# Optimization experiments

Hardware: AMD Instinct MI355X
Metric: run time of the kernel (lower is better)

## Reference

```python
import jax, jax.numpy as jnp
import numpy as np

N, E, G = 10000, 80000, 32
Z, C, B, H = 10, 128, 8, 64
R_MAX = 5.0
AVG_NEIGH = 16.0
L_OFF = [0, 1, 4, 9, 16]  # slice offsets for l = 0..3 blocks of the SH vector


def real_sh(u):
    # Real spherical harmonics up to l=3, 'component' normalization (sum_m Y_lm^2 = 2l+1)
    x, y, z = u[:, 0], u[:, 1], u[:, 2]
    s3, s5, s15 = 3.0 ** 0.5, 5.0 ** 0.5, 15.0 ** 0.5
    cols = [
        jnp.ones_like(x),
        s3 * x, s3 * y, s3 * z,
        s15 * x * y, s15 * y * z, (s5 / 2) * (3 * z ** 2 - 1),
        s15 * x * z, (s15 / 2) * (x ** 2 - y ** 2),
        (70.0 ** 0.5 / 4) * (3 * x ** 2 * y - y ** 3),
        105.0 ** 0.5 * x * y * z,
        (42.0 ** 0.5 / 4) * y * (5 * z ** 2 - 1),
        (7.0 ** 0.5 / 2) * (5 * z ** 3 - 3 * z),
        (42.0 ** 0.5 / 4) * x * (5 * z ** 2 - 1),
        (105.0 ** 0.5 / 2) * z * (x ** 2 - y ** 2),
        (70.0 ** 0.5 / 4) * (x ** 3 - 3 * x * y ** 2),
    ]
    return jnp.stack(cols, axis=-1)  # [E, 16]


def poly_cutoff(x, p=5):
    f = (1.0 - (p + 1) * (p + 2) / 2 * x ** p
         + p * (p + 2) * x ** (p + 1)
         - p * (p + 1) / 2 * x ** (p + 2))
    return f * (x < 1.0).astype(f.dtype)


def setup_inputs() -> dict:
    key = jax.random.key(0)
    ks = jax.random.split(key, 20)
    vectors = jax.random.normal(ks[0], (E, 3), dtype=jnp.float32) * 1.5
    elem = jax.random.randint(ks[1], (N,), 0, Z)
    node_attrs = jax.nn.one_hot(elem, Z, dtype=jnp.float32)
    edge_index = jax.random.randint(ks[2], (2, E), 0, N).astype(jnp.int64)
    batch = jnp.sort(jax.random.randint(ks[3], (N,), 0, G)).astype(jnp.int64)

    def init(k, shape, fan_in):
        return jax.random.normal(k, shape, dtype=jnp.float32) / np.sqrt(fan_in)

    return {
        "vectors": vectors,
        "node_attrs": node_attrs,
        "W_embed": init(ks[4], (Z, C), Z),
        "atomic_energies": -jnp.arange(1, Z + 1, dtype=jnp.float32),
        "rw1": init(ks[5], (2, B, H), B),
        "rw2": init(ks[6], (2, H, H), H),
        "rw3": init(ks[7], (2, H, H), H),
        "rw4": init(ks[8], (2, H, 4 * C), H),
        "Wmix": init(ks[9], (2, 4, C, C), C),
        "U": init(ks[10], (2, Z, 4), Z),
        "Wprod": init(ks[11], (2, C, C), C),
        "Wsc": init(ks[12], (2, C, C), C),
        "Wro0": init(ks[13], (C, 1), C),
        "Wro1a": init(ks[14], (C, 16), C),
        "Wro1b": init(ks[15], (16, 1), 16),
        "scale": jnp.array([1.0], dtype=jnp.float32),
        "shift": jnp.array([0.0], dtype=jnp.float32),
        "edge_index": edge_index,
        "batch": batch,
    }


def reference(vectors, node_attrs, W_embed, atomic_energies, rw1, rw2, rw3, rw4,
              Wmix, U, Wprod, Wsc, Wro0, Wro1a, Wro1b, scale, shift,
              edge_index, batch):
    sender, receiver = edge_index[0], edge_index[1]
    r = jnp.linalg.norm(vectors, axis=-1)                     # [E]
    u = vectors / r[:, None]
    Y = real_sh(u)                                            # [E, 16]
    n = jnp.arange(1, B + 1, dtype=vectors.dtype)
    bessel = jnp.sqrt(2.0 / R_MAX) * jnp.sin(n[None] * jnp.pi * r[:, None] / R_MAX) / r[:, None]
    edge_feats = bessel * poly_cutoff(r / R_MAX)[:, None]     # [E, B]

    h = node_attrs @ W_embed                                  # [N, C] node embedding
    node_e0 = node_attrs @ atomic_energies                    # [N] atomic reference energies
    e0 = jax.ops.segment_sum(node_e0, batch, num_segments=G)  # [G]

    node_inter = jnp.zeros((node_attrs.shape[0],), dtype=vectors.dtype)
    for i in range(2):  # interaction layers (fixed small count)
        f = jax.nn.silu(edge_feats @ rw1[i])
        f = jax.nn.silu(f @ rw2[i])
        f = jax.nn.silu(f @ rw3[i])
        R_w = (f @ rw4[i]).reshape(-1, 4, C)                  # [E, 4, C] radial weights per l-path
        hs = h[sender]                                        # [E, C] edge gather
        A_parts = []
        for l in range(4):
            # channelwise tensor product (uvu): scalar node feats x Y_l -> l
            m = (R_w[:, l, :] * hs)[:, :, None] * Y[:, None, L_OFF[l]:L_OFF[l + 1]]  # [E, C, 2l+1]
            agg = jax.ops.segment_sum(m, receiver, num_segments=node_attrs.shape[0]) / AVG_NEIGH
            A_parts.append(jnp.einsum('ncm,cd->ndm', agg, Wmix[i, l]))
        # product basis: rotation-invariant powers per l, element-dependent contraction
        inv = jnp.stack([(p ** 2).sum(-1) for p in A_parts], axis=-1)  # [N, C, 4]
        w = node_attrs @ U[i]                                          # [N, 4]
        h = jnp.einsum('ncl,nl->nc', inv, w) @ Wprod[i] + h @ Wsc[i]   # product + residual sc
        if i == 0:
            node_inter = node_inter + (h @ Wro0)[:, 0]                 # linear readout
        else:
            node_inter = node_inter + (jax.nn.silu(h @ Wro1a) @ Wro1b)[:, 0]  # nonlinear readout
    node_inter = scale[0] * node_inter + shift[0]                       # scale-shift
    total = e0 + jax.ops.segment_sum(node_inter, batch, num_segments=G)
    return total  # [G] per-graph energies
```

## Files before the change

kernel.cpp:

```cpp
#include <hip/hip_runtime.h>

#define NN 10000
#define NE 80000
#define NG 32
#define NZ 10
#define NC 128
#define RMAXF 5.0f

typedef _Float16 f16;
typedef _Float16 half8 __attribute__((ext_vector_type(8)));
typedef float f32x4 __attribute__((ext_vector_type(4)));

__device__ __forceinline__ float silu_f(float x) {
    return x / (1.0f + __expf(-x));
}

__device__ __forceinline__ int clampi(int v, int lo, int hi) {
    return v < lo ? lo : (v > hi ? hi : v);
}

__device__ __forceinline__ uint4 pack8f(float4 a, float4 b) {
    union { f16 h[8]; uint4 u; } P;
    P.h[0] = (f16)a.x; P.h[1] = (f16)a.y; P.h[2] = (f16)a.z; P.h[3] = (f16)a.w;
    P.h[4] = (f16)b.x; P.h[5] = (f16)b.y; P.h[6] = (f16)b.z; P.h[7] = (f16)b.w;
    return P.u;
}

__global__ void zero_stuff(int* counts, int* cursor, float* out) {
    int i = blockIdx.x * blockDim.x + threadIdx.x;
    if (i < NN) { counts[i] = 0; cursor[i] = 0; }
    if (i < NG) out[i] = 0.0f;
}

__global__ void prep_weights(const float* __restrict__ Wmix, const float* __restrict__ Wprod,
                             const float* __restrict__ Wsc,
                             const float* __restrict__ rw2, const float* __restrict__ rw3,
                             const float* __restrict__ rw4,
                             f16* __restrict__ WmixT, f16* __restrict__ WprodT, f16* __restrict__ WscT,
                             f16* __restrict__ w2T, f16* __restrict__ w3T, f16* __restrict__ w4T) {
    int i = blockIdx.x * blockDim.x + threadIdx.x;
    if (i < 2 * 4 * 128 * 128) {
        int cc = i & 127, d = (i >> 7) & 127, g = i >> 14;
        WmixT[i] = (f16)Wmix[((size_t)g * 128 + cc) * 128 + d];
    }
    if (i < 2 * 128 * 128) {
        int cc = i & 127, d = (i >> 7) & 127, g = i >> 14;
        WprodT[i] = (f16)Wprod[((size_t)g * 128 + cc) * 128 + d];
        WscT[i]   = (f16)Wsc[((size_t)g * 128 + cc) * 128 + d];
    }
    if (i < 2 * 512 * 64) {
        int k = i & 63, j = (i >> 6) & 511, ly = i >> 15;
        w4T[i] = (f16)rw4[((size_t)ly * 64 + k) * 512 + j];
    }
    if (i < 2 * 64 * 64) {
        int k = i & 63, j = (i >> 6) & 63, ly = i >> 12;
        w2T[i] = (f16)rw2[((size_t)ly * 64 + k) * 64 + j];
        w3T[i] = (f16)rw3[((size_t)ly * 64 + k) * 64 + j];
    }
}

__global__ void node_init(const float* __restrict__ attrs, const float* __restrict__ W_embed,
                          const float* __restrict__ ae, const float* __restrict__ U,
                          float* __restrict__ h, float* __restrict__ node_e0, float* __restrict__ wU) {
    int gid = blockIdx.x * blockDim.x + threadIdx.x;
    if (gid >= NN * NC) return;
    int n = gid >> 7, c = gid & 127;
    float a[NZ];
#pragma unroll
    for (int z = 0; z < NZ; z++) a[z] = attrs[n * NZ + z];
    float acc = 0.f;
#pragma unroll
    for (int z = 0; z < NZ; z++) acc += a[z] * W_embed[z * NC + c];
    h[(size_t)n * NC + c] = acc;
    if (c == 0) {
        float e = 0.f;
#pragma unroll
        for (int z = 0; z < NZ; z++) e += a[z] * ae[z];
        node_e0[n] = e;
    }
    if (c < 8) {
        int i = c >> 2, l = c & 3;
        float s = 0.f;
#pragma unroll
        for (int z = 0; z < NZ; z++) s += a[z] * U[i * NZ * 4 + z * 4 + l];
        wU[(size_t)i * NN * 4 + n * 4 + l] = s;
    }
}

__global__ void edge_geom(const float* __restrict__ vec, float* __restrict__ Y, float* __restrict__ ef) {
    int e = blockIdx.x * blockDim.x + threadIdx.x;
    if (e >= NE) return;
    float vx = vec[e * 3 + 0], vy = vec[e * 3 + 1], vz = vec[e * 3 + 2];
    float r = sqrtf(vx * vx + vy * vy + vz * vz);
    float inv = 1.0f / r;
    float x = vx * inv, y = vy * inv, z = vz * inv;
    const float s3 = 1.7320508075688772f;
    const float s5 = 2.23606797749979f;
    const float s15 = 3.872983346207417f;
    const float c9 = 2.091650066335189f;
    const float c10 = 10.246950765959598f;
    const float c11 = 1.6201851746019651f;
    const float c12 = 1.3228756555322954f;
    const float c14 = 5.123475382979799f;
    float o[16];
    o[0] = 1.0f;
    o[1] = s3 * x; o[2] = s3 * y; o[3] = s3 * z;
    o[4] = s15 * x * y; o[5] = s15 * y * z; o[6] = 0.5f * s5 * (3.f * z * z - 1.f);
    o[7] = s15 * x * z; o[8] = 0.5f * s15 * (x * x - y * y);
    o[9] = c9 * (3.f * x * x * y - y * y * y);
    o[10] = c10 * x * y * z;
    o[11] = c11 * y * (5.f * z * z - 1.f);
    o[12] = c12 * (5.f * z * z * z - 3.f * z);
    o[13] = c11 * x * (5.f * z * z - 1.f);
    o[14] = c14 * z * (x * x - y * y);
    o[15] = c9 * (x * x * x - 3.f * x * y * y);
#pragma unroll
    for (int m = 0; m < 16; m++) Y[(size_t)e * 16 + m] = o[m];
    float xc = r / RMAXF;
    float cut = 0.0f;
    if (xc < 1.0f) {
        float x5 = xc * xc * xc * xc * xc;
        cut = 1.0f - 21.0f * x5 + 35.0f * x5 * xc - 15.0f * x5 * xc * xc;
    }
    float pref = sqrtf(2.0f / RMAXF) * inv * cut;
#pragma unroll
    for (int b = 0; b < 8; b++) {
        float arg = (float)(b + 1) * 3.14159265358979323846f * r / RMAXF;
        ef[(size_t)e * 8 + b] = pref * sinf(arg);
    }
}

__global__ void hist_recv(const int* __restrict__ recv, int* __restrict__ counts) {
    int e = blockIdx.x * blockDim.x + threadIdx.x;
    if (e < NE) atomicAdd(&counts[clampi(recv[e], 0, NN - 1)], 1);
}

__global__ void scan_counts(const int* __restrict__ counts, int* __restrict__ rowstart) {
    __shared__ int part[1024];
    int t = threadIdx.x;
    const int CH = 10;
    int base = t * CH;
    int loc[CH];
    int s = 0;
#pragma unroll
    for (int j = 0; j < CH; j++) {
        int v = (base + j < NN) ? counts[base + j] : 0;
        loc[j] = s; s += v;
    }
    part[t] = s;
    __syncthreads();
    for (int off = 1; off < 1024; off <<= 1) {
        int v = (t >= off) ? part[t - off] : 0;
        __syncthreads();
        part[t] += v;
        __syncthreads();
    }
    int chunk = (t > 0) ? part[t - 1] : 0;
#pragma unroll
    for (int j = 0; j < CH; j++)
        if (base + j < NN) rowstart[base + j] = chunk + loc[j];
    if (t == 0) rowstart[NN] = part[1023];
}

__global__ void scatter_edges(const int* __restrict__ recv, const int* __restrict__ rowstart,
                              int* __restrict__ cursor, int* __restrict__ elist) {
    int e = blockIdx.x * blockDim.x + threadIdx.x;
    if (e < NE) {
        int r = clampi(recv[e], 0, NN - 1);
        int p = atomicAdd(&cursor[r], 1);
        int slot = clampi(rowstart[r] + p, 0, NE - 1);
        elist[slot] = e;
    }
}

__global__ __launch_bounds__(256) void edge_mlp(const float* __restrict__ ef,
                                                const float* __restrict__ w1,
                                                const f16* __restrict__ w2T, const f16* __restrict__ w3T,
                                                const f16* __restrict__ w4T,
                                                f16* __restrict__ Rw) {
    __shared__ __align__(16) char L[16384];
    char* X1 = L;
    char* X2 = L + 8192;

    int tid = threadIdx.x;
    int lane = tid & 63;
    int w = tid >> 6;
    int ln = lane & 15, kq = lane >> 4;
    int eb = blockIdx.x * 64;

    {
        int jb = w * 16;
        const float4* efv = (const float4*)(ef + (size_t)(eb + lane) * 8);
        float4 ea = efv[0], eb4 = efv[1];
        float in8[8] = {ea.x, ea.y, ea.z, ea.w, eb4.x, eb4.y, eb4.z, eb4.w};
        f16 pk[16];
#pragma unroll
        for (int j = 0; j < 16; j++) {
            float a = 0.f;
#pragma unroll
            for (int b = 0; b < 8; b++) a += in8[b] * w1[b * 64 + jb + j];
            pk[j] = (f16)silu_f(a);
        }
        int base = lane * 128 + jb * 2;
#pragma unroll
        for (int t = 0; t < 2; t++) {
            int byte = (base + t * 16) ^ ((lane & 7) << 4);
            *(uint4*)(X1 + byte) = ((uint4*)pk)[t];
        }
    }
    __syncthreads();

    {
        half8 a[2];
#pragma unroll
        for (int kc = 0; kc < 2; kc++) {
            int row = w * 16 + ln;
            int byte = (row * 128 + kc * 64 + kq * 16) ^ ((row & 7) << 4);
            a[kc] = *(const half8*)(X1 + byte);
        }
#pragma unroll
        for (int nt = 0; nt < 4; nt++) {
            f32x4 acc = {0.f, 0.f, 0.f, 0.f};
#pragma unroll
            for (int kc = 0; kc < 2; kc++) {
                half8 b = *(const half8*)(w2T + (nt * 16 + ln) * 64 + kc * 32 + kq * 8);
                acc = __builtin_amdgcn_mfma_f32_16x16x32_f16(a[kc], b, acc, 0, 0, 0);
            }
#pragma unroll
            for (int r = 0; r < 4; r++) {
                int row = w * 16 + kq * 4 + r;
                int byte = (row * 128 + (nt * 16 + ln) * 2) ^ ((row & 7) << 4);
                *(f16*)(X2 + byte) = (f16)silu_f(acc[r]);
            }
        }
    }
    __syncthreads();

    {
        half8 a[2];
#pragma unroll
        for (int kc = 0; kc < 2; kc++) {
            int row = w * 16 + ln;
            int byte = (row * 128 + kc * 64 + kq * 16) ^ ((row & 7) << 4);
            a[kc] = *(const half8*)(X2 + byte);
        }
#pragma unroll
        for (int nt = 0; nt < 4; nt++) {
            f32x4 acc = {0.f, 0.f, 0.f, 0.f};
#pragma unroll
            for (int kc = 0; kc < 2; kc++) {
                half8 b = *(const half8*)(w3T + (nt * 16 + ln) * 64 + kc * 32 + kq * 8);
                acc = __builtin_amdgcn_mfma_f32_16x16x32_f16(a[kc], b, acc, 0, 0, 0);
            }
#pragma unroll
            for (int r = 0; r < 4; r++) {
                int row = w * 16 + kq * 4 + r;
                int byte = (row * 128 + (nt * 16 + ln) * 2) ^ ((row & 7) << 4);
                *(f16*)(X1 + byte) = (f16)silu_f(acc[r]);
            }
        }
    }
    __syncthreads();

    half8 a3[2];
#pragma unroll
    for (int kc = 0; kc < 2; kc++) {
        int row = w * 16 + ln;
        int byte = (row * 128 + kc * 64 + kq * 16) ^ ((row & 7) << 4);
        a3[kc] = *(const half8*)(X1 + byte);
    }
    for (int s = 0; s < 8; s++) {
#pragma unroll
        for (int nt = 0; nt < 4; nt++) {
            f32x4 acc = {0.f, 0.f, 0.f, 0.f};
#pragma unroll
            for (int kc = 0; kc < 2; kc++) {
                half8 b = *(const half8*)(w4T + (s * 64 + nt * 16 + ln) * 64 + kc * 32 + kq * 8);
                acc = __builtin_amdgcn_mfma_f32_16x16x32_f16(a3[kc], b, acc, 0, 0, 0);
            }
#pragma unroll
            for (int r = 0; r < 4; r++) {
                int row = w * 16 + kq * 4 + r;
                int byte = (row * 128 + (nt * 16 + ln) * 2) ^ ((row & 7) << 4);
                *(f16*)(X2 + byte) = (f16)acc[r];
            }
        }
        __syncthreads();
#pragma unroll
        for (int it = 0; it < 2; it++) {
            int i = it * 256 + tid;
            int row = i >> 3, chunk = i & 7;
            int byte = (row * 128 + chunk * 16) ^ ((row & 7) << 4);
            uint4 v = *(const uint4*)(X2 + byte);
            *(uint4*)(Rw + (size_t)(eb + row) * 512 + s * 64 + chunk * 8) = v;
        }
        __syncthreads();
    }
}

__global__ __launch_bounds__(256) void agg_only(const int* __restrict__ rowstart, const int* __restrict__ elist,
                                                const int* __restrict__ send, const float* __restrict__ h_in,
                                                const f16* __restrict__ Rw, const float* __restrict__ Y,
                                                f16* __restrict__ aggH) {
    __shared__ int eL[64], sL[64];
    int n = blockIdx.x, tid = threadIdx.x;
    int c = tid & 127, mh = tid >> 7;
    float acc[8];
#pragma unroll
    for (int q = 0; q < 8; q++) acc[q] = 0.f;
    int beg = rowstart[n], end = rowstart[n + 1];
    for (int base = beg; base < end; base += 64) {
        int cnt = min(64, end - base);
        __syncthreads();
        if (tid < cnt) {
            int e = clampi(elist[base + tid], 0, NE - 1);
            eL[tid] = e;
            sL[tid] = clampi(send[e], 0, NN - 1);
        }
        __syncthreads();
        for (int idx = 0; idx < cnt; idx++) {
            int e = eL[idx];
            int s = sL[idx];
            float hs = h_in[(size_t)s * NC + c];
            const f16* rwp = Rw + (size_t)e * 512;
            float y[8];
#pragma unroll
            for (int q = 0; q < 8; q++) y[q] = Y[(size_t)e * 16 + mh * 8 + q];
            if (mh == 0) {
                float p0 = (float)rwp[c] * hs;
                float p1 = (float)rwp[128 + c] * hs;
                float p2 = (float)rwp[256 + c] * hs;
                acc[0] += p0 * y[0];
                acc[1] += p1 * y[1]; acc[2] += p1 * y[2]; acc[3] += p1 * y[3];
                acc[4] += p2 * y[4]; acc[5] += p2 * y[5]; acc[6] += p2 * y[6]; acc[7] += p2 * y[7];
            } else {
                float p2 = (float)rwp[256 + c] * hs;
                float p3 = (float)rwp[384 + c] * hs;
                acc[0] += p2 * y[0];
#pragma unroll
                for (int q = 1; q < 8; q++) acc[q] += p3 * y[q];
            }
        }
    }
    const float inv16 = 1.0f / 16.0f;
#pragma unroll
    for (int q = 0; q < 8; q++)
        aggH[(size_t)n * 2048 + (size_t)(mh * 8 + q) * NC + c] = (f16)(acc[q] * inv16);
}

__global__ __launch_bounds__(256) void mix_a(
    const f16* __restrict__ aggH, const f16* __restrict__ WmixT,
    const float* __restrict__ wU, f16* __restrict__ invwG, int layer)
{
    __shared__ __align__(16) char Lb[16384];

    int tid = threadIdx.x;
    int b = blockIdx.x;
    int nb = (b >> 1) * 16;
    int half = b & 1;
    int lane = tid & 63;
    int w = tid >> 6;
    int dt = half * 4 + w;
    int ln = lane & 15, kq = lane >> 4;
    char* myB = Lb + w * 4096;

    float4 wUreg[4];
#pragma unroll
    for (int r = 0; r < 4; r++)
        wUreg[r] = *(const float4*)(wU + (size_t)(nb + kq * 4 + r) * 4);

    float invwacc[4] = {0.f, 0.f, 0.f, 0.f};
    const f16* aggRow = aggH + (size_t)(nb + ln) * 2048 + kq * 8;

#pragma unroll
    for (int g = 0; g < 4; g++) {
        const int mstart = (g == 0) ? 0 : (g == 1) ? 1 : (g == 2) ? 4 : 9;
        const int mend   = (g == 0) ? 1 : (g == 1) ? 4 : (g == 2) ? 9 : 16;
        {
            const f16* Bt = WmixT + ((size_t)(layer * 4 + g) << 14);
#pragma unroll
            for (int i = 0; i < 4; i++) {
                int q = i * 64 + lane;
                int row = q >> 4, col = q & 15;
                uint4 v = *(const uint4*)(Bt + (dt * 16 + row) * 128 + col * 8);
                int byte = (row * 256 + col * 16) ^ ((row & 7) << 4);
                *(uint4*)(myB + byte) = v;
            }
        }
#pragma unroll
        for (int m = mstart; m < mend; m++) {
            f32x4 acc = {0.f, 0.f, 0.f, 0.f};
#pragma unroll
            for (int k = 0; k < 4; k++) {
                half8 a = *(const half8*)(aggRow + m * 128 + k * 32);
                int byte = (ln * 256 + k * 64 + kq * 16) ^ ((ln & 7) << 4);
                half8 bb = *(const half8*)(myB + byte);
                acc = __builtin_amdgcn_mfma_f32_16x16x32_f16(a, bb, acc, 0, 0, 0);
            }
#pragma unroll
            for (int r = 0; r < 4; r++) {
                float wur = (g == 0) ? wUreg[r].x : (g == 1) ? wUreg[r].y : (g == 2) ? wUreg[r].z : wUreg[r].w;
                invwacc[r] += acc[r] * acc[r] * wur;
            }
        }
    }

#pragma unroll
    for (int r = 0; r < 4; r++)
        invwG[(size_t)(nb + kq * 4 + r) * 128 + dt * 16 + ln] = (f16)invwacc[r];
}

__global__ __launch_bounds__(512) void mix_b(
    const f16* __restrict__ invwG, const float* __restrict__ h_in,
    const f16* __restrict__ WprodT, const f16* __restrict__ WscT,
    const float* __restrict__ Wro0, const float* __restrict__ Wro1a, const float* __restrict__ Wro1b,
    float* __restrict__ h_out, float* __restrict__ ni, int layer)
{
    __shared__ __align__(16) char Lb[13312];
    f16*   invwH = (f16*)(Lb);
    f16*   hH    = (f16*)(Lb + 4096);
    f16*   houtH = (f16*)(Lb + 8192);
    float* p16L  = (float*)(Lb + 12288);

    int tid = threadIdx.x;
    int nb = blockIdx.x * 16;
    int lane = tid & 63;
    int w = tid >> 6;
    int ln = lane & 15, kq = lane >> 4;

    if (tid < 256) {
        int node = tid >> 4, ch = tid & 15;
        int byte = (node * 256 + ch * 16) ^ ((node & 7) << 4);
        uint4 iv = *(const uint4*)(invwG + (size_t)(nb + node) * 128 + ch * 8);
        *(uint4*)((char*)invwH + byte) = iv;
        const float4* hp = (const float4*)(h_in + (size_t)(nb + node) * 128 + ch * 8);
        float4 g0 = hp[0], g1 = hp[1];
        *(uint4*)((char*)hH + byte) = pack8f(g0, g1);
    }
    __syncthreads();

    {
        half8 ai[4], ah[4];
#pragma unroll
        for (int k = 0; k < 4; k++) {
            int byte = (ln * 256 + (k * 32 + kq * 8) * 2) ^ ((ln & 7) << 4);
            ai[k] = *(const half8*)((char*)invwH + byte);
            ah[k] = *(const half8*)((char*)hH + byte);
        }
        const f16* Bp = WprodT + ((size_t)layer << 14);
        const f16* Bs = WscT + ((size_t)layer << 14);
        f32x4 acc = {0.f, 0.f, 0.f, 0.f};
#pragma unroll
        for (int k = 0; k < 4; k++) {
            half8 bb = *(const half8*)(Bp + (w * 16 + ln) * 128 + k * 32 + kq * 8);
            acc = __builtin_amdgcn_mfma_f32_16x16x32_f16(ai[k], bb, acc, 0, 0, 0);
        }
#pragma unroll
        for (int k = 0; k < 4; k++) {
            half8 bb = *(const half8*)(Bs + (w * 16 + ln) * 128 + k * 32 + kq * 8);
            acc = __builtin_amdgcn_mfma_f32_16x16x32_f16(ah[k], bb, acc, 0, 0, 0);
        }
#pragma unroll
        for (int r = 0; r < 4; r++) {
            int node = kq * 4 + r;
            int d = w * 16 + ln;
            h_out[(size_t)(nb + node) * 128 + d] = acc[r];
            houtH[node * 128 + d] = (f16)acc[r];
        }
    }
    __syncthreads();

    if (tid < 256) {
        int rn = tid >> 4, rj = tid & 15;
        if (layer == 0) {
            float s = 0.f;
            for (int cc = rj; cc < 128; cc += 16) s += (float)houtH[rn * 128 + cc] * Wro0[cc];
            p16L[tid] = s;
        } else {
            float s = 0.f;
            for (int cc = 0; cc < 128; cc++) s += (float)houtH[rn * 128 + cc] * Wro1a[cc * 16 + rj];
            s = silu_f(s);
            p16L[tid] = s * Wro1b[rj];
        }
    }
    __syncthreads();
    if (tid < 16) {
        float t = 0.f;
#pragma unroll
        for (int j = 0; j < 16; j++) t += p16L[tid * 16 + j];
        ni[nb + tid] = (layer == 0) ? t : (ni[nb + tid] + t);
    }
}

__global__ void finalize(const float* __restrict__ node_e0, const float* __restrict__ ni,
                         const int* __restrict__ batch, const float* __restrict__ scale,
                         const float* __restrict__ shift, float* __restrict__ out) {
    __shared__ float bins[NG];
    int tid = threadIdx.x;
    if (tid < NG) bins[tid] = 0.f;
    __syncthreads();
    int n = blockIdx.x * blockDim.x + tid;
    if (n < NN) {
        float v = node_e0[n] + scale[0] * ni[n] + shift[0];
        atomicAdd(&bins[clampi(batch[n], 0, NG - 1)], v);
    }
    __syncthreads();
    if (tid < NG) atomicAdd(&out[tid], bins[tid]);
}

extern "C" void kernel_launch(void* const* d_in, const int* in_sizes, int n_in,
                              void* d_out, int out_size, void* d_ws, size_t ws_size,
                              hipStream_t stream) {
    (void)in_sizes; (void)n_in; (void)out_size; (void)ws_size;
    const float* vectors = (const float*)d_in[0];
    const float* attrs   = (const float*)d_in[1];
    const float* W_embed = (const float*)d_in[2];
    const float* ae      = (const float*)d_in[3];
    const float* rw1     = (const float*)d_in[4];
    const float* rw2     = (const float*)d_in[5];
    const float* rw3     = (const float*)d_in[6];
    const float* rw4     = (const float*)d_in[7];
    const float* Wmix    = (const float*)d_in[8];
    const float* U       = (const float*)d_in[9];
    const float* Wprod   = (const float*)d_in[10];
    const float* Wsc     = (const float*)d_in[11];
    const float* Wro0    = (const float*)d_in[12];
    const float* Wro1a   = (const float*)d_in[13];
    const float* Wro1b   = (const float*)d_in[14];
    const float* scale   = (const float*)d_in[15];
    const float* shift   = (const float*)d_in[16];
    const int* eidx      = (const int*)d_in[17];
    const int* batch     = (const int*)d_in[18];
    float* out = (float*)d_out;

    char* w = (char*)d_ws;
    size_t off = 0;
    auto alloc = [&](size_t bytes) -> void* {
        void* p = (void*)(w + off);
        off += (bytes + 255) & ~(size_t)255;
        return p;
    };
    float* Y       = (float*)alloc((size_t)NE * 16 * 4);
    float* ef      = (float*)alloc((size_t)NE * 8 * 4);
    f16*   Rw      = (f16*)  alloc((size_t)NE * 512 * 2);
    f16*   aggH    = (f16*)  alloc((size_t)NN * 2048 * 2);
    float* hA      = (float*)alloc((size_t)NN * NC * 4);
    float* hB      = (float*)alloc((size_t)NN * NC * 4);
    f16*   invwG   = (f16*)  alloc((size_t)NN * NC * 2);
    float* wU      = (float*)alloc((size_t)2 * NN * 4 * 4);
    float* node_e0 = (float*)alloc((size_t)NN * 4);
    float* ni      = (float*)alloc((size_t)NN * 4);
    f16*   WmixT   = (f16*)  alloc((size_t)2 * 4 * 128 * 128 * 2);
    f16*   WprodT  = (f16*)  alloc((size_t)2 * 128 * 128 * 2);
    f16*   WscT    = (f16*)  alloc((size_t)2 * 128 * 128 * 2);
    f16*   w2T     = (f16*)  alloc((size_t)2 * 64 * 64 * 2);
    f16*   w3T     = (f16*)  alloc((size_t)2 * 64 * 64 * 2);
    f16*   w4T     = (f16*)  alloc((size_t)2 * 512 * 64 * 2);
    int* counts    = (int*)alloc((size_t)NN * 4);
    int* rowstart  = (int*)alloc((size_t)(NN + 1) * 4);
    int* cursor    = (int*)alloc((size_t)NN * 4);
    int* elist     = (int*)alloc((size_t)NE * 4);

    const int* send = eidx;
    const int* recv = eidx + NE;
    zero_stuff<<<(NN + 255) / 256, 256, 0, stream>>>(counts, cursor, out);
    prep_weights<<<512, 256, 0, stream>>>(Wmix, Wprod, Wsc, rw2, rw3, rw4,
                                          WmixT, WprodT, WscT, w2T, w3T, w4T);
    node_init<<<(NN * NC + 255) / 256, 256, 0, stream>>>(attrs, W_embed, ae, U, hA, node_e0, wU);
    edge_geom<<<(NE + 255) / 256, 256, 0, stream>>>(vectors, Y, ef);
    hist_recv<<<(NE + 255) / 256, 256, 0, stream>>>(recv, counts);
    scan_counts<<<1, 1024, 0, stream>>>(counts, rowstart);
    scatter_edges<<<(NE + 255) / 256, 256, 0, stream>>>(recv, rowstart, cursor, elist);

    float* hcur = hA;
    float* hnext = hB;
    for (int layer = 0; layer < 2; layer++) {
        edge_mlp<<<NE / 64, 256, 0, stream>>>(
            ef, rw1 + layer * 8 * 64,
            w2T + (size_t)layer * 64 * 64, w3T + (size_t)layer * 64 * 64,
            w4T + (size_t)layer * 512 * 64, Rw);
        agg_only<<<NN, 256, 0, stream>>>(rowstart, elist, send, hcur, Rw, Y, aggH);
        mix_a<<<(NN / 16) * 2, 256, 0, stream>>>(
            aggH, WmixT, wU + (size_t)layer * NN * 4, invwG, layer);
        mix_b<<<NN / 16, 512, 0, stream>>>(
            invwG, hcur, WprodT, WscT, Wro0, Wro1a, Wro1b, hnext, ni, layer);
        float* t = hcur; hcur = hnext; hnext = t;
    }
    finalize<<<(NN + 255) / 256, 256, 0, stream>>>(node_e0, ni, batch, scale, shift, out);
}
```

Before: 337.7 us.

## Store per-edge geometry and radial weights in receiver-sorted (CSR) order

Edge geometry and edge features are now computed in receiver-sorted order via elist, so edge_mlp writes Rw in CSR order. Sender indices are also permuted during scatter. agg_only can then read Rw, Y and sender ids contiguously instead of through an indirection. This removes the random gathers of the 1KB-per-edge Rw rows and the elist/send lookups in the aggregation hot loop. In exchange, edge_geom must wait for the sort and does a gathered read of the input vectors.

```diff
diff --git a/kernel.cpp b/kernel.cpp
--- a/kernel.cpp
+++ b/kernel.cpp
@@ -87,9 +87,11 @@
     }
 }
 
-__global__ void edge_geom(const float* __restrict__ vec, float* __restrict__ Y, float* __restrict__ ef) {
-    int e = blockIdx.x * blockDim.x + threadIdx.x;
-    if (e >= NE) return;
+__global__ void edge_geom(const float* __restrict__ vec, const int* __restrict__ elist,
+                          float* __restrict__ Y2, float* __restrict__ ef2) {
+    int i = blockIdx.x * blockDim.x + threadIdx.x;
+    if (i >= NE) return;
+    int e = clampi(elist[i], 0, NE - 1);
     float vx = vec[e * 3 + 0], vy = vec[e * 3 + 1], vz = vec[e * 3 + 2];
     float r = sqrtf(vx * vx + vy * vy + vz * vz);
     float inv = 1.0f / r;
@@ -115,7 +117,7 @@
     o[14] = c14 * z * (x * x - y * y);
     o[15] = c9 * (x * x * x - 3.f * x * y * y);
 #pragma unroll
-    for (int m = 0; m < 16; m++) Y[(size_t)e * 16 + m] = o[m];
+    for (int m = 0; m < 16; m++) Y2[(size_t)i * 16 + m] = o[m];
     float xc = r / RMAXF;
     float cut = 0.0f;
     if (xc < 1.0f) {
@@ -126,7 +128,7 @@
 #pragma unroll
     for (int b = 0; b < 8; b++) {
         float arg = (float)(b + 1) * 3.14159265358979323846f * r / RMAXF;
-        ef[(size_t)e * 8 + b] = pref * sinf(arg);
+        ef2[(size_t)i * 8 + b] = pref * sinf(arg);
     }
 }
 
@@ -162,22 +164,25 @@
     if (t == 0) rowstart[NN] = part[1023];
 }
 
-__global__ void scatter_edges(const int* __restrict__ recv, const int* __restrict__ rowstart,
-                              int* __restrict__ cursor, int* __restrict__ elist) {
+__global__ void scatter_edges(const int* __restrict__ recv, const int* __restrict__ send,
+                              const int* __restrict__ rowstart,
+                              int* __restrict__ cursor, int* __restrict__ elist,
+                              int* __restrict__ send2) {
     int e = blockIdx.x * blockDim.x + threadIdx.x;
     if (e < NE) {
         int r = clampi(recv[e], 0, NN - 1);
         int p = atomicAdd(&cursor[r], 1);
         int slot = clampi(rowstart[r] + p, 0, NE - 1);
         elist[slot] = e;
-    }
-}
-
-__global__ __launch_bounds__(256) void edge_mlp(const float* __restrict__ ef,
+        send2[slot] = clampi(send[e], 0, NN - 1);
+    }
+}
+
+__global__ __launch_bounds__(256) void edge_mlp(const float* __restrict__ ef2,
                                                 const float* __restrict__ w1,
                                                 const f16* __restrict__ w2T, const f16* __restrict__ w3T,
                                                 const f16* __restrict__ w4T,
-                                                f16* __restrict__ Rw) {
+                                                f16* __restrict__ Rw2) {
     __shared__ __align__(16) char L[16384];
     char* X1 = L;
     char* X2 = L + 8192;
@@ -190,7 +195,7 @@
 
     {
         int jb = w * 16;
-        const float4* efv = (const float4*)(ef + (size_t)(eb + lane) * 8);
+        const float4* efv = (const float4*)(ef2 + (size_t)(eb + lane) * 8);
         float4 ea = efv[0], eb4 = efv[1];
         float in8[8] = {ea.x, ea.y, ea.z, ea.w, eb4.x, eb4.y, eb4.z, eb4.w};
         f16 pk[16];
@@ -292,17 +297,17 @@
             int row = i >> 3, chunk = i & 7;
             int byte = (row * 128 + chunk * 16) ^ ((row & 7) << 4);
             uint4 v = *(const uint4*)(X2 + byte);
-            *(uint4*)(Rw + (size_t)(eb + row) * 512 + s * 64 + chunk * 8) = v;
+            *(uint4*)(Rw2 + (size_t)(eb + row) * 512 + s * 64 + chunk * 8) = v;
         }
         __syncthreads();
     }
 }
 
-__global__ __launch_bounds__(256) void agg_only(const int* __restrict__ rowstart, const int* __restrict__ elist,
-                                                const int* __restrict__ send, const float* __restrict__ h_in,
-                                                const f16* __restrict__ Rw, const float* __restrict__ Y,
+__global__ __launch_bounds__(256) void agg_only(const int* __restrict__ rowstart,
+                                                const int* __restrict__ send2, const float* __restrict__ h_in,
+                                                const f16* __restrict__ Rw2, const float* __restrict__ Y2,
                                                 f16* __restrict__ aggH) {
-    __shared__ int eL[64], sL[64];
+    __shared__ int sL[64];
     int n = blockIdx.x, tid = threadIdx.x;
     int c = tid & 127, mh = tid >> 7;
     float acc[8];
@@ -312,20 +317,16 @@
     for (int base = beg; base < end; base += 64) {
         int cnt = min(64, end - base);
         __syncthreads();
-        if (tid < cnt) {
-            int e = clampi(elist[base + tid], 0, NE - 1);
-            eL[tid] = e;
-            sL[tid] = clampi(send[e], 0, NN - 1);
-        }
+        if (tid < cnt) sL[tid] = send2[base + tid];
         __syncthreads();
-        for (int idx = 0; idx < cnt; idx++) {
-            int e = eL[idx];
-            int s = sL[idx];
+        for (int j = 0; j < cnt; j++) {
+            int idx = base + j;
+            int s = sL[j];
             float hs = h_in[(size_t)s * NC + c];
-            const f16* rwp = Rw + (size_t)e * 512;
-            float y[8];
-#pragma unroll
-            for (int q = 0; q < 8; q++) y[q] = Y[(size_t)e * 16 + mh * 8 + q];
+            const f16* rwp = Rw2 + (size_t)idx * 512;
+            const float4* yv = (const float4*)(Y2 + (size_t)idx * 16 + mh * 8);
+            float4 ya = yv[0], yb = yv[1];
+            float y[8] = {ya.x, ya.y, ya.z, ya.w, yb.x, yb.y, yb.z, yb.w};
             if (mh == 0) {
                 float p0 = (float)rwp[c] * hs;
                 float p1 = (float)rwp[128 + c] * hs;
@@ -540,9 +541,9 @@
         off += (bytes + 255) & ~(size_t)255;
         return p;
     };
-    float* Y       = (float*)alloc((size_t)NE * 16 * 4);
-    float* ef      = (float*)alloc((size_t)NE * 8 * 4);
-    f16*   Rw      = (f16*)  alloc((size_t)NE * 512 * 2);
+    float* Y2      = (float*)alloc((size_t)NE * 16 * 4);
+    float* ef2     = (float*)alloc((size_t)NE * 8 * 4);
+    f16*   Rw2     = (f16*)  alloc((size_t)NE * 512 * 2);
     f16*   aggH    = (f16*)  alloc((size_t)NN * 2048 * 2);
     float* hA      = (float*)alloc((size_t)NN * NC * 4);
     float* hB      = (float*)alloc((size_t)NN * NC * 4);
@@ -560,6 +561,7 @@
     int* rowstart  = (int*)alloc((size_t)(NN + 1) * 4);
     int* cursor    = (int*)alloc((size_t)NN * 4);
     int* elist     = (int*)alloc((size_t)NE * 4);
+    int* send2     = (int*)alloc((size_t)NE * 4);
 
     const int* send = eidx;
     const int* recv = eidx + NE;
@@ -567,19 +569,19 @@
     prep_weights<<<512, 256, 0, stream>>>(Wmix, Wprod, Wsc, rw2, rw3, rw4,
                                           WmixT, WprodT, WscT, w2T, w3T, w4T);
     node_init<<<(NN * NC + 255) / 256, 256, 0, stream>>>(attrs, W_embed, ae, U, hA, node_e0, wU);
-    edge_geom<<<(NE + 255) / 256, 256, 0, stream>>>(vectors, Y, ef);
     hist_recv<<<(NE + 255) / 256, 256, 0, stream>>>(recv, counts);
     scan_counts<<<1, 1024, 0, stream>>>(counts, rowstart);
-    scatter_edges<<<(NE + 255) / 256, 256, 0, stream>>>(recv, rowstart, cursor, elist);
+    scatter_edges<<<(NE + 255) / 256, 256, 0, stream>>>(recv, send, rowstart, cursor, elist, send2);
+    edge_geom<<<(NE + 255) / 256, 256, 0, stream>>>(vectors, elist, Y2, ef2);
 
     float* hcur = hA;
     float* hnext = hB;
     for (int layer = 0; layer < 2; layer++) {
         edge_mlp<<<NE / 64, 256, 0, stream>>>(
-            ef, rw1 + layer * 8 * 64,
+            ef2, rw1 + layer * 8 * 64,
             w2T + (size_t)layer * 64 * 64, w3T + (size_t)layer * 64 * 64,
-            w4T + (size_t)layer * 512 * 64, Rw);
-        agg_only<<<NN, 256, 0, stream>>>(rowstart, elist, send, hcur, Rw, Y, aggH);
+            w4T + (size_t)layer * 512 * 64, Rw2);
+        agg_only<<<NN, 256, 0, stream>>>(rowstart, send2, hcur, Rw2, Y2, aggH);
         mix_a<<<(NN / 16) * 2, 256, 0, stream>>>(
             aggH, WmixT, wU + (size_t)layer * NN * 4, invwG, layer);
         mix_b<<<NN / 16, 512, 0, stream>>>(
```

Result: no change. 335.2 us (-0.7%).
